# Kernel optimization log

Measured on AMD Instinct MI355X. Metric: run time of the kernel, lower is better.

The kernel has to match this reference:

```python
import jax, jax.numpy as jnp
import numpy as np

WORD_VOCAB, WORD_DIM = 50257, 512
CHAR_VOCAB, CHAR_DIM = 262, 128
OUT_DIM = 1024
B, SW, SC = 32, 256, 16
EMB_DIM = WORD_DIM + CHAR_DIM


def setup_inputs() -> dict:
    key = jax.random.key(0)
    ks = jax.random.split(key, 12)
    word_inputs = jax.random.randint(ks[0], (B, SW), 0, WORD_VOCAB)
    char_ids = jax.random.randint(ks[1], (B, SW, SC), 0, CHAR_VOCAB)
    char_lengths = jax.random.randint(ks[2], (B, SW), 1, SC + 1)  # at least 1 char
    word_table = jax.random.normal(ks[3], (WORD_VOCAB, WORD_DIM), jnp.float32) * 0.02
    char_table = jax.random.normal(ks[4], (CHAR_VOCAB, CHAR_DIM), jnp.float32) * 0.02
    # RecursiveCell: gate = Linear(2d -> 3d), project = Linear(2d -> d)
    Wg = jax.random.normal(ks[5], (3 * CHAR_DIM, 2 * CHAR_DIM), jnp.float32) * (1.0 / np.sqrt(2 * CHAR_DIM))
    bg = jnp.zeros((3 * CHAR_DIM,), jnp.float32)
    Wp = jax.random.normal(ks[6], (CHAR_DIM, 2 * CHAR_DIM), jnp.float32) * (1.0 / np.sqrt(2 * CHAR_DIM))
    bp = jnp.zeros((CHAR_DIM,), jnp.float32)
    # final projection Linear(emb_dim -> output_dim)
    W_out = jax.random.normal(ks[7], (OUT_DIM, EMB_DIM), jnp.float32) * (1.0 / np.sqrt(EMB_DIM))
    b_out = jnp.zeros((OUT_DIM,), jnp.float32)
    return {"word_inputs": word_inputs, "char_ids": char_ids, "char_lengths": char_lengths,
            "word_table": word_table, "char_table": char_table,
            "Wg": Wg, "bg": bg, "Wp": Wp, "bp": bp, "W_out": W_out, "b_out": b_out}


def reference(word_inputs, char_ids, char_lengths, word_table, char_table, Wg, bg, Wp, bp, W_out, b_out):
    b, sw = word_inputs.shape
    sc = char_ids.shape[-1]
    d = char_table.shape[-1]
    n = b * sw

    word_emb = word_table[word_inputs]                      # [B, SW, WORD_DIM]

    ids = char_ids.reshape(n, sc)
    lens = char_lengths.reshape(n, 1)
    layer0 = char_table[ids]                                # [N, SC, d]
    pos = jnp.arange(sc)

    def step(layer, length):
        # vectorized RecursiveCell over all adjacent pairs i in [0, SC-2]
        left = layer[:, :-1, :]                             # [N, SC-1, d]
        right = layer[:, 1:, :]                             # [N, SC-1, d]
        flat = jnp.concatenate([left, right], axis=-1)      # [N, SC-1, 2d]
        z = flat @ Wp.T + bp                                # [N, SC-1, d]
        g = jax.nn.softmax((flat @ Wg.T + bg).reshape(n, sc - 1, 3, d), axis=2)
        ret = g[:, :, 0] * left + g[:, :, 1] * right + g[:, :, 2] * z
        new_layer = jnp.pad(ret, ((0, 0), (0, 1), (0, 0)))  # positions >= SC-1 stay zero
        # masked_scatter_: update position i iff i < len - length
        mask = (pos[None, :] < (lens - length))[..., None]  # [N, SC, 1]
        return jnp.where(mask, new_layer, layer), None

    layer, _ = jax.lax.scan(step, layer0, jnp.arange(1, sc))
    char_repr = layer[:, 0, :].reshape(b, sw, d)            # [B, SW, d]

    token_embedding = jnp.concatenate([word_emb, char_repr], axis=-1)
    return token_embedding @ W_out.T + b_out                # [B, SW, OUT_DIM]
```

## Files before the change

### kernel.cpp

```cpp
#include <hip/hip_runtime.h>
#include <hip/hip_bf16.h>

#define NTOK 8192
#define SCC  16
#define CD   128
#define WD   512
#define OD   1024
#define ED   640
#define TW   4
#define LOG2E 1.4426950408889634f

typedef __attribute__((ext_vector_type(8))) short short8;
typedef __attribute__((ext_vector_type(4))) float f32x4;

#if defined(__has_builtin)
#  if __has_builtin(__builtin_amdgcn_exp2f)
#    define EXP2(x) __builtin_amdgcn_exp2f(x)
#  else
#    define EXP2(x) exp2f(x)
#  endif
#else
#  define EXP2(x) exp2f(x)
#endif

__device__ __forceinline__ unsigned short f2bf(float f) {
    union { float f; unsigned u; } v; v.f = f;
    unsigned r = v.u + 0x7FFF + ((v.u >> 16) & 1);
    return (unsigned short)(r >> 16);
}

__device__ __forceinline__ unsigned short f2bf_fast(float f) {
    unsigned r;
    asm("v_cvt_pk_bf16_f32 %0, %1, %2" : "=v"(r) : "v"(f), "v"(f));
    return (unsigned short)r;
}

__global__ void sort_zero(int* s) { if (threadIdx.x < 48) s[threadIdx.x] = 0; }

__global__ void sort_hist(const int* __restrict__ lengths, int* __restrict__ s) {
    const int i = blockIdx.x * 256 + threadIdx.x;
    if (i < NTOK) atomicAdd(&s[lengths[i] - 1], 1);
}

__global__ void sort_prefix(int* s) {
    if (threadIdx.x == 0) {
        int acc = 0;
        for (int b = 15; b >= 0; --b) { s[16 + b] = acc; acc += s[b]; }
    }
}

__global__ __launch_bounds__(256) void sort_scatter_det(
    const int* __restrict__ lengths, int* __restrict__ s)
{
    __shared__ int wsum[4];
    __shared__ int running;
    const int b   = blockIdx.x;
    const int tid = threadIdx.x;
    if (tid == 0) running = s[16 + b];
    __syncthreads();
    for (int c0 = 0; c0 < NTOK; c0 += 256) {
        const int i = c0 + tid;
        const bool f = (lengths[i] - 1 == b);
        const unsigned long long m = __ballot(f);
        const int wv = tid >> 6;
        if ((tid & 63) == 0) wsum[wv] = __popcll(m);
        __syncthreads();
        int excl = 0;
#pragma unroll
        for (int k = 0; k < 4; ++k) if (k < wv) excl += wsum[k];
        const int lanerank = __popcll(m & ((1ull << (tid & 63)) - 1ull));
        if (f) s[48 + running + excl + lanerank] = i;
        const int tot = wsum[0] + wsum[1] + wsum[2] + wsum[3];
        __syncthreads();
        if (tid == 0) running += tot;
        __syncthreads();
    }
}

__global__ __launch_bounds__(256) void pack_weights(
    const float* __restrict__ Wg, const float* __restrict__ Wp,
    uint4* __restrict__ packed)
{
    const int gid  = blockIdx.x * 256 + threadIdx.x;
    const int lane = gid & 63;
    const int kf   = (gid >> 6) & 7;
    const int c    = (gid >> 9) & 3;
    const int w    = (gid >> 11) & 7;
    const int n    = c * 128 + w * 16 + (lane & 15);
    const int k0   = kf * 32 + (lane >> 4) * 8;
    const float sc = (n < 384) ? LOG2E : 1.0f;
    const float* src = (n < 384) ? (Wg + n * 256 + k0) : (Wp + (n - 384) * 256 + k0);
    uint4 o;
    o.x = f2bf(src[0] * sc) | ((unsigned)f2bf(src[1] * sc) << 16);
    o.y = f2bf(src[2] * sc) | ((unsigned)f2bf(src[3] * sc) << 16);
    o.z = f2bf(src[4] * sc) | ((unsigned)f2bf(src[5] * sc) << 16);
    o.w = f2bf(src[6] * sc) | ((unsigned)f2bf(src[7] * sc) << 16);
    packed[gid] = o;
}

__global__ __launch_bounds__(256) void pack_wout(
    const float* __restrict__ W_out, uint4* __restrict__ packed)
{
    const int gid  = blockIdx.x * 256 + threadIdx.x;
    const int lane = gid & 63;
    const int kf   = (gid >> 6) % 20;
    const int nb   = (gid >> 6) / 20;
    const int n    = nb * 16 + (lane & 15);
    const int k0   = kf * 32 + (lane >> 4) * 8;
    const float* src = W_out + (size_t)n * ED + k0;
    uint4 o;
    o.x = f2bf(src[0]) | ((unsigned)f2bf(src[1]) << 16);
    o.y = f2bf(src[2]) | ((unsigned)f2bf(src[3]) << 16);
    o.z = f2bf(src[4]) | ((unsigned)f2bf(src[5]) << 16);
    o.w = f2bf(src[6]) | ((unsigned)f2bf(src[7]) << 16);
    packed[gid] = o;
}

#define LOAD_B(DST, KF)                                                     \
    {                                                                       \
        const uint4* wp_ = Wpacked + (w * 32 + (KF)) * 64 + lane;           \
        union { uint4 u; short8 s; } cv0, cv1, cv2, cv3;                    \
        cv0.u = wp_[0];    DST[0] = cv0.s;                                  \
        cv1.u = wp_[512];  DST[1] = cv1.s;                                  \
        cv2.u = wp_[1024]; DST[2] = cv2.s;                                  \
        cv3.u = wp_[1536]; DST[3] = cv3.s;                                  \
    }

#define LOAD_B_LDS(DST, KFI)                                                \
    {                                                                       \
        const uint4* sp_ = SW + ((w * 3 + (KFI)) * 4) * 64 + lane;          \
        union { uint4 u; short8 s; } d0, d1, d2, d3;                        \
        d0.u = sp_[0];   DST[0] = d0.s;                                     \
        d1.u = sp_[64];  DST[1] = d1.s;                                     \
        d2.u = sp_[128]; DST[2] = d2.s;                                     \
        d3.u = sp_[192]; DST[3] = d3.s;                                     \
    }

#define MFMA_PHASE(BV, KF)                                                  \
    {                                                                       \
        _Pragma("unroll")                                                   \
        for (int m_ = 0; m_ < 4; ++m_) {                                    \
            if (m_ < mfrags) {                                              \
                const int r_ = m_ * 16 + col + (((KF) >= 4) ? 4 : 0);       \
                int ba_ = (r_ << 8) + (((KF) & 3) << 6) + (q << 4);         \
                ba_ ^= (r_ & 15) << 4;                                      \
                const short8 a_ = *reinterpret_cast<const short8*>(Xc + ba_); \
                acc[m_][0] = __builtin_amdgcn_mfma_f32_16x16x32_bf16(a_, BV[0], acc[m_][0], 0, 0, 0); \
                acc[m_][1] = __builtin_amdgcn_mfma_f32_16x16x32_bf16(a_, BV[1], acc[m_][1], 0, 0, 0); \
                acc[m_][2] = __builtin_amdgcn_mfma_f32_16x16x32_bf16(a_, BV[2], acc[m_][2], 0, 0, 0); \
                acc[m_][3] = __builtin_amdgcn_mfma_f32_16x16x32_bf16(a_, BV[3], acc[m_][3], 0, 0, 0); \
            }                                                               \
        }                                                                   \
    }

__global__ __launch_bounds__(512, 2) void scan_mfma(
    const int*   __restrict__ char_ids,
    const int*   __restrict__ char_lengths,
    const float* __restrict__ char_table,
    const float* __restrict__ bg, const float* __restrict__ bp,
    const uint4* __restrict__ Wpacked,
    const int*   __restrict__ order,
    unsigned short* __restrict__ char_repr)
{
    __shared__ __align__(16) unsigned short X[2 * 68 * 128];
    __shared__ __align__(16) uint4 SW[8 * 3 * 4 * 64];
    __shared__ int toksh[TW];
    __shared__ int Lsh[TW];

    const int tid  = threadIdx.x;
    const int lane = tid & 63;
    const int w    = tid >> 6;
    const int col  = lane & 15;
    const int q    = lane >> 4;

    if (tid < TW) {
        const int tok = order[blockIdx.x * TW + tid];
        toksh[tid] = tok;
        Lsh[tid]   = char_lengths[tok];
    }

    const int dj = w * 16 + col;
    const float b02 = (bg[dj] - bg[256 + dj]) * LOG2E;
    const float b12 = (bg[128 + dj] - bg[256 + dj]) * LOG2E;
    const float bz  = bp[dj];

    short8 bpin0[4], bpin1[4];
    LOAD_B(bpin0, 0);
    LOAD_B(bpin1, 1);

#pragma unroll
    for (int kfi = 0; kfi < 3; ++kfi)
#pragma unroll
        for (int c = 0; c < 4; ++c)
            SW[((w * 3 + kfi) * 4 + c) * 64 + lane] =
                Wpacked[(w * 32 + c * 8 + (2 + kfi)) * 64 + lane];

    __syncthreads();

    int L[TW];
#pragma unroll
    for (int i = 0; i < TW; ++i) L[i] = Lsh[i];
    const int maxL = max(max(L[0], L[1]), max(L[2], L[3]));

    float stv[4][4];
#pragma unroll
    for (int m = 0; m < 4; ++m) {
        const int p = m * 4 + q;
#pragma unroll
        for (int i = 0; i < 4; ++i) {
            const int id = char_ids[toksh[i] * SCC + p];
            stv[m][i] = char_table[id * CD + dj];
        }
    }

#pragma unroll
    for (int xb = 0; xb < 2; ++xb) {
        char* Xb = reinterpret_cast<char*>(X) + xb * 17408;
#pragma unroll
        for (int m = 0; m < 4; ++m)
#pragma unroll
            for (int i = 0; i < 4; ++i) {
                const int rl = m * 16 + q * 4 + i;
                int bl = (rl << 8) + (dj << 1);
                bl ^= (rl & 15) << 4;
                *reinterpret_cast<unsigned short*>(Xb + bl) = f2bf_fast(stv[m][i]);
            }
    }
    for (int i2 = tid; i2 < 2 * 4 * 64; i2 += 512) {
        const int xb = i2 >> 8;
        const int r  = 64 + ((i2 >> 6) & 3), ku = i2 & 63;
        int ba = (r << 8) + (ku << 2);
        ba ^= (r & 15) << 4;
        *reinterpret_cast<unsigned*>(reinterpret_cast<char*>(X) + xb * 17408 + ba) = 0u;
    }
    __syncthreads();

    int cur = 0;
    for (int len = 1; len < maxL; ++len) {
        const int Amax   = maxL - len;
        const int mfrags = ((4 * Amax + 15) >> 4);
        const int mf_w0  = (Amax + 4) >> 2;
        const int mf_w   = (mf_w0 < 4) ? mf_w0 : 4;

        const char* Xc = reinterpret_cast<const char*>(X) + cur * 17408;
        char*       Xn = reinterpret_cast<char*>(X) + (cur ^ 1) * 17408;

        f32x4 acc[4][4];
#pragma unroll
        for (int m = 0; m < 4; ++m)
#pragma unroll
            for (int c = 0; c < 4; ++c) acc[m][c] = (f32x4){0.f, 0.f, 0.f, 0.f};

        short8 bA[4], bB[4], bL[4];
        LOAD_B(bA, 5);
        LOAD_B(bB, 6);
        MFMA_PHASE(bpin0, 0);
        LOAD_B_LDS(bL, 0);
        MFMA_PHASE(bpin1, 1);
        MFMA_PHASE(bL, 2);
        LOAD_B_LDS(bL, 1);
        MFMA_PHASE(bL, 3);
        LOAD_B_LDS(bL, 2);
        MFMA_PHASE(bL, 4);
        MFMA_PHASE(bA, 5);
        LOAD_B(bA, 7);
        MFMA_PHASE(bB, 6);
        MFMA_PHASE(bA, 7);

        float shifted[5][4];
#pragma unroll
        for (int m = 0; m < 4; ++m) {
            if (m <= mfrags) {
#pragma unroll
                for (int i = 0; i < 4; ++i)
                    shifted[m][i] = __shfl(stv[m][i], (lane + 16) & 63);
            }
        }
#pragma unroll
        for (int i = 0; i < 4; ++i) shifted[4][i] = 0.f;

#pragma unroll
        for (int m = 0; m < 4; ++m) {
            if (m < mfrags) {
                const int p = m * 4 + q;
#pragma unroll
                for (int i = 0; i < 4; ++i) {
                    const float a0  = acc[m][0][i];
                    const float a1  = acc[m][1][i];
                    const float a2v = acc[m][2][i];
                    const float z   = acc[m][3][i] + bz;
                    const float E0  = EXP2(a0 - a2v + b02);
                    const float E1  = EXP2(a1 - a2v + b12);
                    const float left  = stv[m][i];
                    const float right = (q < 3) ? shifted[m][i] : shifted[m + 1][i];
                    const float inv = __builtin_amdgcn_rcpf(E0 + E1 + 1.0f);
                    const float nv  = (E0 * left + E1 * right + z) * inv;
                    stv[m][i] = (p < L[i] - len) ? nv : stv[m][i];
                }
            }
        }

#pragma unroll
        for (int m = 0; m < 4; ++m) {
            if (m < mf_w) {
#pragma unroll
                for (int i = 0; i < 4; ++i) {
                    const int rl = m * 16 + q * 4 + i;
                    int bl = (rl << 8) + (dj << 1);
                    bl ^= (rl & 15) << 4;
                    *reinterpret_cast<unsigned short*>(Xn + bl) = f2bf_fast(stv[m][i]);
                }
            }
        }
        __syncthreads();
        cur ^= 1;
    }

    if (q == 0) {
#pragma unroll
        for (int i = 0; i < 4; ++i)
            char_repr[toksh[i] * CD + dj] = f2bf_fast(stv[0][i]);
    }
}

#define TPB2 32

__global__ __launch_bounds__(512) void out_mfma(
    const int*   __restrict__ word_inputs,
    const float* __restrict__ word_table,
    const unsigned short* __restrict__ char_repr,
    const uint4* __restrict__ pwout,
    const float* __restrict__ b_out,
    float*       __restrict__ out)
{
    __shared__ __align__(16) unsigned short E[TPB2 * ED];

    const int tg   = blockIdx.x * TPB2;
    const int tid  = threadIdx.x;
    const int lane = tid & 63;
    const int w    = tid >> 6;
    const int col  = lane & 15;
    const int q    = lane >> 4;

    for (int i = tid; i < TPB2 * 256; i += 512) {
        const int rt = i >> 8, kp = i & 255;
        const float2 v = *reinterpret_cast<const float2*>(
            word_table + (size_t)word_inputs[tg + rt] * WD + 2 * kp);
        const unsigned u = f2bf(v.x) | ((unsigned)f2bf(v.y) << 16);
        int baddr = rt * 1280 + kp * 4;
        baddr ^= (rt & 7) << 4;
        *reinterpret_cast<unsigned*>(reinterpret_cast<char*>(E) + baddr) = u;
    }
    for (int i = tid; i < TPB2 * 64; i += 512) {
        const int rt = i >> 6, kp = i & 63;
        const unsigned u = *reinterpret_cast<const unsigned*>(
            char_repr + (tg + rt) * CD + 2 * kp);
        int baddr = rt * 1280 + 1024 + kp * 4;
        baddr ^= (rt & 7) << 4;
        *reinterpret_cast<unsigned*>(reinterpret_cast<char*>(E) + baddr) = u;
    }
    __syncthreads();

    f32x4 acc[2][8];
#pragma unroll
    for (int mm = 0; mm < 2; ++mm)
#pragma unroll
        for (int nf = 0; nf < 8; ++nf) acc[mm][nf] = (f32x4){0.f, 0.f, 0.f, 0.f};

#pragma unroll 4
    for (int kf = 0; kf < 20; ++kf) {
        short8 a[2];
#pragma unroll
        for (int mm = 0; mm < 2; ++mm) {
            const int row = mm * 16 + col;
            int ba = row * 1280 + kf * 64 + q * 16;
            ba ^= (row & 7) << 4;
            a[mm] = *reinterpret_cast<const short8*>(
                reinterpret_cast<const char*>(E) + ba);
        }
#pragma unroll
        for (int nf = 0; nf < 8; ++nf) {
            const int nb = w * 8 + nf;
            union { uint4 u; short8 s; } cv;
            cv.u = pwout[(nb * 20 + kf) * 64 + lane];
            acc[0][nf] = __builtin_amdgcn_mfma_f32_16x16x32_bf16(a[0], cv.s, acc[0][nf], 0, 0, 0);
            acc[1][nf] = __builtin_amdgcn_mfma_f32_16x16x32_bf16(a[1], cv.s, acc[1][nf], 0, 0, 0);
        }
    }

#pragma unroll
    for (int nf = 0; nf < 8; ++nf) {
        const int j = (w * 8 + nf) * 16 + col;
        const float bias = b_out[j];
#pragma unroll
        for (int mm = 0; mm < 2; ++mm)
#pragma unroll
            for (int i = 0; i < 4; ++i) {
                out[(size_t)(tg + mm * 16 + q * 4 + i) * OD + j] = acc[mm][nf][i] + bias;
            }
    }
}


extern "C" void kernel_launch(void* const* d_in, const int* in_sizes, int n_in,
                              void* d_out, int out_size, void* d_ws, size_t ws_size,
                              hipStream_t stream)
{
    const int*   word_inputs  = (const int*)  d_in[0];
    const int*   char_ids     = (const int*)  d_in[1];
    const int*   char_lengths = (const int*)  d_in[2];
    const float* word_table   = (const float*)d_in[3];
    const float* char_table   = (const float*)d_in[4];
    const float* Wg           = (const float*)d_in[5];
    const float* bg           = (const float*)d_in[6];
    const float* Wp           = (const float*)d_in[7];
    const float* bp           = (const float*)d_in[8];
    const float* W_out        = (const float*)d_in[9];
    const float* b_out        = (const float*)d_in[10];

    float* out = (float*)d_out;
    char* ws = (char*)d_ws;
    unsigned short* char_repr = (unsigned short*)ws;
    uint4* Wpacked = (uint4*)(ws + 2 * 1024 * 1024);
    int*   sortbuf = (int*)(ws + 2 * 1024 * 1024 + 256 * 1024);
    const int* order = sortbuf + 48;
    uint4* pwout = (uint4*)(ws + 2 * 1024 * 1024 + 256 * 1024 + 64 * 1024);

    pack_weights<<<64, 256, 0, stream>>>(Wg, Wp, Wpacked);
    pack_wout<<<320, 256, 0, stream>>>(W_out, pwout);
    sort_zero<<<1, 64, 0, stream>>>(sortbuf);
    sort_hist<<<NTOK / 256, 256, 0, stream>>>(char_lengths, sortbuf);
    sort_prefix<<<1, 64, 0, stream>>>(sortbuf);
    sort_scatter_det<<<16, 256, 0, stream>>>(char_lengths, sortbuf);

    scan_mfma<<<NTOK / TW, 512, 0, stream>>>(char_ids, char_lengths, char_table,
                                             bg, bp, Wpacked, order, char_repr);
    out_mfma<<<NTOK / TPB2, 512, 0, stream>>>(word_inputs, word_table, char_repr,
                                              pwout, b_out, out);
}
```

Measured before the change: 260.8 us.

## Single-buffer X tile, pin more weight fragments in registers and LDS

```diff
diff --git a/kernel.cpp b/kernel.cpp
--- a/kernel.cpp
+++ b/kernel.cpp
@@ -128,7 +128,7 @@
 
 #define LOAD_B_LDS(DST, KFI)                                                \
     {                                                                       \
-        const uint4* sp_ = SW + ((w * 3 + (KFI)) * 4) * 64 + lane;          \
+        const uint4* sp_ = SW + ((w * 4 + (KFI)) * 4) * 64 + lane;          \
         union { uint4 u; short8 s; } d0, d1, d2, d3;                        \
         d0.u = sp_[0];   DST[0] = d0.s;                                     \
         d1.u = sp_[64];  DST[1] = d1.s;                                     \
@@ -162,8 +162,8 @@
     const int*   __restrict__ order,
     unsigned short* __restrict__ char_repr)
 {
-    __shared__ __align__(16) unsigned short X[2 * 68 * 128];
-    __shared__ __align__(16) uint4 SW[8 * 3 * 4 * 64];
+    __shared__ __align__(16) unsigned short X[68 * 128];
+    __shared__ __align__(16) uint4 SW[8 * 4 * 4 * 64];
     __shared__ int toksh[TW];
     __shared__ int Lsh[TW];
 
@@ -184,15 +184,17 @@
     const float b12 = (bg[128 + dj] - bg[256 + dj]) * LOG2E;
     const float bz  = bp[dj];
 
-    short8 bpin0[4], bpin1[4];
+    short8 bpin0[4], bpin1[4], bpin6[4], bpin7[4];
     LOAD_B(bpin0, 0);
     LOAD_B(bpin1, 1);
-
-#pragma unroll
-    for (int kfi = 0; kfi < 3; ++kfi)
+    LOAD_B(bpin6, 6);
+    LOAD_B(bpin7, 7);
+
+#pragma unroll
+    for (int kfi = 0; kfi < 4; ++kfi)
 #pragma unroll
         for (int c = 0; c < 4; ++c)
-            SW[((w * 3 + kfi) * 4 + c) * 64 + lane] =
+            SW[((w * 4 + kfi) * 4 + c) * 64 + lane] =
                 Wpacked[(w * 32 + c * 8 + (2 + kfi)) * 64 + lane];
 
     __syncthreads();
@@ -213,37 +215,30 @@
         }
     }
 
-#pragma unroll
-    for (int xb = 0; xb < 2; ++xb) {
-        char* Xb = reinterpret_cast<char*>(X) + xb * 17408;
-#pragma unroll
-        for (int m = 0; m < 4; ++m)
-#pragma unroll
-            for (int i = 0; i < 4; ++i) {
-                const int rl = m * 16 + q * 4 + i;
-                int bl = (rl << 8) + (dj << 1);
-                bl ^= (rl & 15) << 4;
-                *reinterpret_cast<unsigned short*>(Xb + bl) = f2bf_fast(stv[m][i]);
-            }
-    }
-    for (int i2 = tid; i2 < 2 * 4 * 64; i2 += 512) {
-        const int xb = i2 >> 8;
-        const int r  = 64 + ((i2 >> 6) & 3), ku = i2 & 63;
+    char* Xc = reinterpret_cast<char*>(X);
+#pragma unroll
+    for (int m = 0; m < 4; ++m)
+#pragma unroll
+        for (int i = 0; i < 4; ++i) {
+            const int rl = m * 16 + q * 4 + i;
+            int bl = (rl << 8) + (dj << 1);
+            bl ^= (rl & 15) << 4;
+            *reinterpret_cast<unsigned short*>(Xc + bl) = f2bf_fast(stv[m][i]);
+        }
+    {
+        const int r = 64 + (tid >> 7), ku = tid & 63;
+    }
+    for (int i2 = tid; i2 < 4 * 64; i2 += 512) {
+        const int r = 64 + (i2 >> 6), ku = i2 & 63;
         int ba = (r << 8) + (ku << 2);
         ba ^= (r & 15) << 4;
-        *reinterpret_cast<unsigned*>(reinterpret_cast<char*>(X) + xb * 17408 + ba) = 0u;
+        *reinterpret_cast<unsigned*>(Xc + ba) = 0u;
     }
     __syncthreads();
 
-    int cur = 0;
     for (int len = 1; len < maxL; ++len) {
         const int Amax   = maxL - len;
         const int mfrags = ((4 * Amax + 15) >> 4);
-        const int mf_w0  = (Amax + 4) >> 2;
-        const int mf_w   = (mf_w0 < 4) ? mf_w0 : 4;
-
-        const char* Xc = reinterpret_cast<const char*>(X) + cur * 17408;
-        char*       Xn = reinterpret_cast<char*>(X) + (cur ^ 1) * 17408;
 
         f32x4 acc[4][4];
 #pragma unroll
@@ -251,21 +246,19 @@
 #pragma unroll
             for (int c = 0; c < 4; ++c) acc[m][c] = (f32x4){0.f, 0.f, 0.f, 0.f};
 
-        short8 bA[4], bB[4], bL[4];
-        LOAD_B(bA, 5);
-        LOAD_B(bB, 6);
+        short8 bL[4];
+        LOAD_B_LDS(bL, 0);
         MFMA_PHASE(bpin0, 0);
-        LOAD_B_LDS(bL, 0);
         MFMA_PHASE(bpin1, 1);
         MFMA_PHASE(bL, 2);
         LOAD_B_LDS(bL, 1);
         MFMA_PHASE(bL, 3);
         LOAD_B_LDS(bL, 2);
         MFMA_PHASE(bL, 4);
-        MFMA_PHASE(bA, 5);
-        LOAD_B(bA, 7);
-        MFMA_PHASE(bB, 6);
-        MFMA_PHASE(bA, 7);
+        LOAD_B_LDS(bL, 3);
+        MFMA_PHASE(bL, 5);
+        MFMA_PHASE(bpin6, 6);
+        MFMA_PHASE(bpin7, 7);
 
         float shifted[5][4];
 #pragma unroll
@@ -299,21 +292,21 @@
                 }
             }
         }
+        __syncthreads();
 
 #pragma unroll
         for (int m = 0; m < 4; ++m) {
-            if (m < mf_w) {
+            if (m < mfrags) {
 #pragma unroll
                 for (int i = 0; i < 4; ++i) {
                     const int rl = m * 16 + q * 4 + i;
                     int bl = (rl << 8) + (dj << 1);
                     bl ^= (rl & 15) << 4;
-                    *reinterpret_cast<unsigned short*>(Xn + bl) = f2bf_fast(stv[m][i]);
+                    *reinterpret_cast<unsigned short*>(Xc + bl) = f2bf_fast(stv[m][i]);
                 }
             }
         }
         __syncthreads();
-        cur ^= 1;
     }
 
     if (q == 0) {
```

Measured after the change: 264.8 us. Within noise of the previous version (+1.6%).

## Process two token groups per block sharing B-fragment loads in recursive scan

Applied to the files above, without the earlier changes.

```diff
diff --git a/kernel.cpp b/kernel.cpp
--- a/kernel.cpp
+++ b/kernel.cpp
@@ -7,7 +7,7 @@
 #define WD   512
 #define OD   1024
 #define ED   640
-#define TW   4
+#define TW   8
 #define LOG2E 1.4426950408889634f
 
 typedef __attribute__((ext_vector_type(8))) short short8;
@@ -136,19 +136,72 @@
         d3.u = sp_[192]; DST[3] = d3.s;                                     \
     }
 
-#define MFMA_PHASE(BV, KF)                                                  \
+#define JPH(BV, KF, MB, MF)                                                 \
     {                                                                       \
         _Pragma("unroll")                                                   \
-        for (int m_ = 0; m_ < 4; ++m_) {                                    \
-            if (m_ < mfrags) {                                              \
-                const int r_ = m_ * 16 + col + (((KF) >= 4) ? 4 : 0);       \
+        for (int m_ = 0; m_ < 2; ++m_) {                                    \
+            if (m_ < (MF)) {                                                \
+                const int r_ = ((MB) + m_) * 16 + col + (((KF) >= 4) ? 4 : 0); \
                 int ba_ = (r_ << 8) + (((KF) & 3) << 6) + (q << 4);         \
                 ba_ ^= (r_ & 15) << 4;                                      \
-                const short8 a_ = *reinterpret_cast<const short8*>(Xc + ba_); \
-                acc[m_][0] = __builtin_amdgcn_mfma_f32_16x16x32_bf16(a_, BV[0], acc[m_][0], 0, 0, 0); \
-                acc[m_][1] = __builtin_amdgcn_mfma_f32_16x16x32_bf16(a_, BV[1], acc[m_][1], 0, 0, 0); \
-                acc[m_][2] = __builtin_amdgcn_mfma_f32_16x16x32_bf16(a_, BV[2], acc[m_][2], 0, 0, 0); \
-                acc[m_][3] = __builtin_amdgcn_mfma_f32_16x16x32_bf16(a_, BV[3], acc[m_][3], 0, 0, 0); \
+                const short8 aA_ = *reinterpret_cast<const short8*>(Xa + ba_); \
+                accA[m_][0] = __builtin_amdgcn_mfma_f32_16x16x32_bf16(aA_, BV[0], accA[m_][0], 0, 0, 0); \
+                accA[m_][1] = __builtin_amdgcn_mfma_f32_16x16x32_bf16(aA_, BV[1], accA[m_][1], 0, 0, 0); \
+                accA[m_][2] = __builtin_amdgcn_mfma_f32_16x16x32_bf16(aA_, BV[2], accA[m_][2], 0, 0, 0); \
+                accA[m_][3] = __builtin_amdgcn_mfma_f32_16x16x32_bf16(aA_, BV[3], accA[m_][3], 0, 0, 0); \
+                const short8 aB_ = *reinterpret_cast<const short8*>(Xb + ba_); \
+                accB[m_][0] = __builtin_amdgcn_mfma_f32_16x16x32_bf16(aB_, BV[0], accB[m_][0], 0, 0, 0); \
+                accB[m_][1] = __builtin_amdgcn_mfma_f32_16x16x32_bf16(aB_, BV[1], accB[m_][1], 0, 0, 0); \
+                accB[m_][2] = __builtin_amdgcn_mfma_f32_16x16x32_bf16(aB_, BV[2], accB[m_][2], 0, 0, 0); \
+                accB[m_][3] = __builtin_amdgcn_mfma_f32_16x16x32_bf16(aB_, BV[3], accB[m_][3], 0, 0, 0); \
+            }                                                               \
+        }                                                                   \
+    }
+
+#define JOINT_PASS(MB, MF)                                                  \
+    {                                                                       \
+        short8 b0[4], b1[4], bL[4];                                         \
+        LOAD_B(b0, 0);                                                      \
+        LOAD_B(b1, 1);                                                      \
+        JPH(b0, 0, MB, MF);                                                 \
+        LOAD_B(b0, 5);                                                      \
+        JPH(b1, 1, MB, MF);                                                 \
+        LOAD_B(b1, 6);                                                      \
+        LOAD_B_LDS(bL, 0);                                                  \
+        JPH(bL, 2, MB, MF);                                                 \
+        LOAD_B_LDS(bL, 1);                                                  \
+        JPH(bL, 3, MB, MF);                                                 \
+        LOAD_B_LDS(bL, 2);                                                  \
+        JPH(bL, 4, MB, MF);                                                 \
+        JPH(b0, 5, MB, MF);                                                 \
+        LOAD_B(b0, 7);                                                      \
+        JPH(b1, 6, MB, MF);                                                 \
+        JPH(b0, 7, MB, MF);                                                 \
+    }
+
+#define COMBINE(STV, LARR, ACC, MB, MF)                                     \
+    {                                                                       \
+        _Pragma("unroll")                                                   \
+        for (int m_ = 0; m_ < 2; ++m_) {                                    \
+            if (m_ < (MF)) {                                                \
+                const int gm_ = (MB) + m_;                                  \
+                const int p_  = gm_ * 4 + q;                                \
+                _Pragma("unroll")                                           \
+                for (int i = 0; i < 4; ++i) {                               \
+                    const float a0  = ACC[m_][0][i];                        \
+                    const float a1  = ACC[m_][1][i];                        \
+                    const float a2v = ACC[m_][2][i];                        \
+                    const float z   = ACC[m_][3][i] + bz;                   \
+                    const float E0  = EXP2(a0 - a2v + b02);                 \
+                    const float E1  = EXP2(a1 - a2v + b12);                 \
+                    const float shf  = __shfl(STV[gm_][i], (lane + 16) & 63); \
+                    const float shfn = (gm_ < 3) ? __shfl(STV[gm_ + 1][i], (lane + 16) & 63) : 0.f; \
+                    const float left  = STV[gm_][i];                        \
+                    const float right = (q < 3) ? shf : shfn;               \
+                    const float inv = __builtin_amdgcn_rcpf(E0 + E1 + 1.0f); \
+                    const float nv  = (E0 * left + E1 * right + z) * inv;   \
+                    STV[gm_][i] = (p_ < LARR[i] - len) ? nv : STV[gm_][i];  \
+                }                                                           \
             }                                                               \
         }                                                                   \
     }
@@ -184,10 +237,6 @@
     const float b12 = (bg[128 + dj] - bg[256 + dj]) * LOG2E;
     const float bz  = bp[dj];
 
-    short8 bpin0[4], bpin1[4];
-    LOAD_B(bpin0, 0);
-    LOAD_B(bpin1, 1);
-
 #pragma unroll
     for (int kfi = 0; kfi < 3; ++kfi)
 #pragma unroll
@@ -197,35 +246,40 @@
 
     __syncthreads();
 
-    int L[TW];
-#pragma unroll
-    for (int i = 0; i < TW; ++i) L[i] = Lsh[i];
-    const int maxL = max(max(L[0], L[1]), max(L[2], L[3]));
-
-    float stv[4][4];
+    int LA[4], LB[4], tokA[4], tokB[4];
+#pragma unroll
+    for (int i = 0; i < 4; ++i) {
+        LA[i] = Lsh[i];     tokA[i] = toksh[i];
+        LB[i] = Lsh[4 + i]; tokB[i] = toksh[4 + i];
+    }
+    int maxL = Lsh[0];
+#pragma unroll
+    for (int j = 1; j < TW; ++j) maxL = max(maxL, Lsh[j]);
+
+    float stvA[4][4], stvB[4][4];
 #pragma unroll
     for (int m = 0; m < 4; ++m) {
         const int p = m * 4 + q;
 #pragma unroll
         for (int i = 0; i < 4; ++i) {
-            const int id = char_ids[toksh[i] * SCC + p];
-            stv[m][i] = char_table[id * CD + dj];
-        }
-    }
-
-#pragma unroll
-    for (int xb = 0; xb < 2; ++xb) {
-        char* Xb = reinterpret_cast<char*>(X) + xb * 17408;
-#pragma unroll
-        for (int m = 0; m < 4; ++m)
-#pragma unroll
-            for (int i = 0; i < 4; ++i) {
-                const int rl = m * 16 + q * 4 + i;
-                int bl = (rl << 8) + (dj << 1);
-                bl ^= (rl & 15) << 4;
-                *reinterpret_cast<unsigned short*>(Xb + bl) = f2bf_fast(stv[m][i]);
-            }
-    }
+            stvA[m][i] = char_table[char_ids[tokA[i] * SCC + p] * CD + dj];
+            stvB[m][i] = char_table[char_ids[tokB[i] * SCC + p] * CD + dj];
+        }
+    }
+
+    char* Xa = reinterpret_cast<char*>(X);
+    char* Xb = reinterpret_cast<char*>(X) + 17408;
+
+#pragma unroll
+    for (int m = 0; m < 4; ++m)
+#pragma unroll
+        for (int i = 0; i < 4; ++i) {
+            const int rl = m * 16 + q * 4 + i;
+            int bl = (rl << 8) + (dj << 1);
+            bl ^= (rl & 15) << 4;
+            *reinterpret_cast<unsigned short*>(Xa + bl) = f2bf_fast(stvA[m][i]);
+            *reinterpret_cast<unsigned short*>(Xb + bl) = f2bf_fast(stvB[m][i]);
+        }
     for (int i2 = tid; i2 < 2 * 4 * 64; i2 += 512) {
         const int xb = i2 >> 8;
         const int r  = 64 + ((i2 >> 6) & 3), ku = i2 & 63;
@@ -235,91 +289,62 @@
     }
     __syncthreads();
 
-    int cur = 0;
     for (int len = 1; len < maxL; ++len) {
         const int Amax   = maxL - len;
         const int mfrags = ((4 * Amax + 15) >> 4);
-        const int mf_w0  = (Amax + 4) >> 2;
-        const int mf_w   = (mf_w0 < 4) ? mf_w0 : 4;
-
-        const char* Xc = reinterpret_cast<const char*>(X) + cur * 17408;
-        char*       Xn = reinterpret_cast<char*>(X) + (cur ^ 1) * 17408;
-
-        f32x4 acc[4][4];
-#pragma unroll
-        for (int m = 0; m < 4; ++m)
-#pragma unroll
-            for (int c = 0; c < 4; ++c) acc[m][c] = (f32x4){0.f, 0.f, 0.f, 0.f};
-
-        short8 bA[4], bB[4], bL[4];
-        LOAD_B(bA, 5);
-        LOAD_B(bB, 6);
-        MFMA_PHASE(bpin0, 0);
-        LOAD_B_LDS(bL, 0);
-        MFMA_PHASE(bpin1, 1);
-        MFMA_PHASE(bL, 2);
-        LOAD_B_LDS(bL, 1);
-        MFMA_PHASE(bL, 3);
-        LOAD_B_LDS(bL, 2);
-        MFMA_PHASE(bL, 4);
-        MFMA_PHASE(bA, 5);
-        LOAD_B(bA, 7);
-        MFMA_PHASE(bB, 6);
-        MFMA_PHASE(bA, 7);
-
-        float shifted[5][4];
-#pragma unroll
-        for (int m = 0; m < 4; ++m) {
-            if (m <= mfrags) {
-#pragma unroll
-                for (int i = 0; i < 4; ++i)
-                    shifted[m][i] = __shfl(stv[m][i], (lane + 16) & 63);
-            }
-        }
-#pragma unroll
-        for (int i = 0; i < 4; ++i) shifted[4][i] = 0.f;
+        const int mf1    = (mfrags < 2) ? mfrags : 2;
+        const int mf2    = mfrags - mf1;
+
+        {
+            f32x4 accA[2][4], accB[2][4];
+#pragma unroll
+            for (int m = 0; m < 2; ++m)
+#pragma unroll
+                for (int c = 0; c < 4; ++c) {
+                    accA[m][c] = (f32x4){0.f, 0.f, 0.f, 0.f};
+                    accB[m][c] = (f32x4){0.f, 0.f, 0.f, 0.f};
+                }
+            JOINT_PASS(0, mf1);
+            COMBINE(stvA, LA, accA, 0, mf1);
+            COMBINE(stvB, LB, accB, 0, mf1);
+        }
+        if (mf2 > 0) {
+            f32x4 accA[2][4], accB[2][4];
+#pragma unroll
+            for (int m = 0; m < 2; ++m)
+#pragma unroll
+                for (int c = 0; c < 4; ++c) {
+                    accA[m][c] = (f32x4){0.f, 0.f, 0.f, 0.f};
+                    accB[m][c] = (f32x4){0.f, 0.f, 0.f, 0.f};
+                }
+            JOINT_PASS(2, mf2);
+            COMBINE(stvA, LA, accA, 2, mf2);
+            COMBINE(stvB, LB, accB, 2, mf2);
+        }
+        __syncthreads();
 
 #pragma unroll
         for (int m = 0; m < 4; ++m) {
             if (m < mfrags) {
-                const int p = m * 4 + q;
-#pragma unroll
-                for (int i = 0; i < 4; ++i) {
-                    const float a0  = acc[m][0][i];
-                    const float a1  = acc[m][1][i];
-                    const float a2v = acc[m][2][i];
-                    const float z   = acc[m][3][i] + bz;
-                    const float E0  = EXP2(a0 - a2v + b02);
-                    const float E1  = EXP2(a1 - a2v + b12);
-                    const float left  = stv[m][i];
-                    const float right = (q < 3) ? shifted[m][i] : shifted[m + 1][i];
-                    const float inv = __builtin_amdgcn_rcpf(E0 + E1 + 1.0f);
-                    const float nv  = (E0 * left + E1 * right + z) * inv;
-                    stv[m][i] = (p < L[i] - len) ? nv : stv[m][i];
-                }
-            }
-        }
-
-#pragma unroll
-        for (int m = 0; m < 4; ++m) {
-            if (m < mf_w) {
 #pragma unroll
                 for (int i = 0; i < 4; ++i) {
                     const int rl = m * 16 + q * 4 + i;
                     int bl = (rl << 8) + (dj << 1);
                     bl ^= (rl & 15) << 4;
-                    *reinterpret_cast<unsigned short*>(Xn + bl) = f2bf_fast(stv[m][i]);
+                    *reinterpret_cast<unsigned short*>(Xa + bl) = f2bf_fast(stvA[m][i]);
+                    *reinterpret_cast<unsigned short*>(Xb + bl) = f2bf_fast(stvB[m][i]);
                 }
             }
         }
         __syncthreads();
-        cur ^= 1;
     }
 
     if (q == 0) {
 #pragma unroll
-        for (int i = 0; i < 4; ++i)
-            char_repr[toksh[i] * CD + dj] = f2bf_fast(stv[0][i]);
+        for (int i = 0; i < 4; ++i) {
+            char_repr[tokA[i] * CD + dj] = f2bf_fast(stvA[0][i]);
+            char_repr[tokB[i] * CD + dj] = f2bf_fast(stvB[0][i]);
+        }
     }
 }
 
```

Result: no change. 266.0 us (+2.0%).
